# Kernel tuning notes

Hardware: AMD Instinct MI355X
Metric: run time of the kernel (lower is better)

Reference implementation:

```python
import jax, jax.numpy as jnp
import numpy as np
from jax import lax

TAU_REF_HOURS = 1.0
INIT_NOISE_SCALE = 0.01
MAX_GROWTH_RATE = 0.3
B, T, N, D = 2, 64, 512, 256


def setup_inputs() -> dict:
    key = jax.random.key(0)
    ks = jax.random.split(key, 8)
    return {
        "x": jax.random.normal(ks[0], (B, T, N, D), dtype=jnp.float32),
        "dt": jax.random.uniform(ks[1], (B, T), dtype=jnp.float32),
        "eps": jax.random.normal(ks[2], (B, T, N, D), dtype=jnp.float32),
        "u_raw_re": jax.random.normal(ks[3], (D, D), dtype=jnp.float32) * 0.02,
        "u_raw_im": jax.random.normal(ks[4], (D, D), dtype=jnp.float32) * 0.02,
        "lam_re": jax.random.normal(ks[5], (D,), dtype=jnp.float32) * 0.01,
        "lam_im": jax.random.normal(ks[6], (D,), dtype=jnp.float32) * 0.1,
        "noise_raw": jax.random.normal(ks[7], (D,), dtype=jnp.float32) * 0.02,
    }


def reference(x, dt, eps, u_raw_re, u_raw_im, lam_re, lam_im, noise_raw):
    # Unitary basis from QR of complex raw matrix (ComplexSVDTransform._unitary_from_raw)
    u, _ = jnp.linalg.qr(lax.complex(u_raw_re, u_raw_im))  # [D, D] complex

    # encode: x @ conj(u)
    x_enc = jnp.einsum("btnd,de->btne", x.astype(jnp.complex64), jnp.conj(u))

    # effective lambda: lam_re -> -softplus(-lam_re), clamped at -max_growth_rate
    lam_r = jnp.maximum(-jax.nn.softplus(-lam_re), -MAX_GROWTH_RATE)
    lam = lax.complex(lam_r, lam_im)  # [D]

    # continuous decay / forcing operators per (b, t, d)
    exp_arg = (dt / TAU_REF_HOURS)[..., None] * lam  # [B, T, D]
    decay = jnp.exp(exp_arg)
    lam_safe = lam + (1e-8 * jnp.sign(lam_r + 1e-12)).astype(lam.dtype)
    forcing = (decay - 1.0) / lam_safe  # expm1(arg)/lam_safe

    # SDE noise: eps * sqrt(dt) * softplus(noise_raw) * init_noise_scale
    dt_scale = jnp.sqrt(jnp.maximum(dt, 0.0))[:, :, None, None]  # [B,T,1,1]
    n_scale = jax.nn.softplus(noise_raw) * INIT_NOISE_SCALE  # [D]
    noise = eps.astype(jnp.complex64) * (dt_scale * n_scale).astype(jnp.complex64)

    # linear recurrence h_t = decay_t * h_{t-1} + forcing_t * x_enc_t + noise_t
    b_term = forcing[:, :, None, :] * x_enc + noise  # [B,T,N,D]
    a_term = jnp.broadcast_to(decay[:, :, None, :], b_term.shape)

    def combine(e1, e2):
        a1, b1 = e1
        a2, b2 = e2
        return (a2 * a1, a2 * b1 + b2)

    _, h = lax.associative_scan(combine, (a_term, b_term), axis=1)  # [B,T,N,D]

    # decode: h @ u
    y = jnp.einsum("btnd,de->btne", h, u)
    return jnp.stack([y.real, y.imag])  # [2,B,T,N,D] float32
```

## Files before the change

kernel.cpp:

```cpp
#include <hip/hip_runtime.h>
#include <math.h>

#define B_ 2
#define T_ 64
#define N_ 512
#define D_ 256
#define M_ (B_*T_*N_)
#define PLANE ((size_t)M_*D_)

typedef unsigned short u16;
typedef __attribute__((ext_vector_type(8))) short bf16x8;
typedef __attribute__((ext_vector_type(4))) float f32x4;

__device__ __forceinline__ u16 f2bf(float f) {
  union { float f; unsigned u; } cv; cv.f = f;
  unsigned u = cv.u;
  return (u16)((u + 0x7FFFu + ((u >> 16) & 1u)) >> 16);
}
__device__ __forceinline__ float bf2f(u16 h) {
  union { unsigned u; float f; } cv; cv.u = ((unsigned)h) << 16;
  return cv.f;
}

__device__ __forceinline__ float wredsum(float x) {
  x += __uint_as_float(__builtin_amdgcn_update_dpp(0u, __float_as_uint(x), 0x111, 0xf, 0xf, true));
  x += __uint_as_float(__builtin_amdgcn_update_dpp(0u, __float_as_uint(x), 0x112, 0xf, 0xf, true));
  x += __uint_as_float(__builtin_amdgcn_update_dpp(0u, __float_as_uint(x), 0x114, 0xf, 0xf, true));
  x += __uint_as_float(__builtin_amdgcn_update_dpp(0u, __float_as_uint(x), 0x118, 0xf, 0xf, true));
  x += __uint_as_float(__builtin_amdgcn_update_dpp(0u, __float_as_uint(x), 0x142, 0xa, 0xf, true));
  x += __uint_as_float(__builtin_amdgcn_update_dpp(0u, __float_as_uint(x), 0x143, 0xc, 0xf, true));
  return __uint_as_float(__builtin_amdgcn_readlane(__float_as_uint(x), 63));
}
__device__ __forceinline__ float lanebcast(float x, int l) {
  return __uint_as_float(__builtin_amdgcn_readlane(__float_as_uint(x), l));
}

template<int P>
__global__ __launch_bounds__(1024, 1) void qr_megastep(
    const float* __restrict__ ure_raw, const float* __restrict__ uim_raw,
    float2* __restrict__ A, float2* __restrict__ tau)
{
  const int tid = threadIdx.x, lane = tid & 63, w = tid >> 6;
  const int role = blockIdx.x;
  __shared__ float2 sv32[32][256];
  __shared__ float2 sfin[32][256];
  __shared__ float2 snext[2][256];
  __shared__ float2 stau2[2];
  __shared__ float2 stau32[32];
  __shared__ float2 stauOut[32];

  constexpr int J0P  = (P > 0) ? 32*(P-1) : 0;
  constexpr int RP   = 256 - J0P;
  constexpr int MCHP = (RP + 63) >> 6;
  constexpr int PIV  = (P == 0) ? 0 : 32;
  constexpr int J0W  = (P == 0) ? 0 : J0P;
  constexpr int RW   = 256 - J0W;
  constexpr int MCHW = (RW + 63) >> 6;

  if constexpr (P == 0) {
    if (role > 0) {
      const int c0 = 32*role;
      const int c = tid & 31, r0 = tid >> 5;
      #pragma unroll
      for (int r8 = 0; r8 < 8; ++r8) {
        int r = r0 + r8*32;
        A[(size_t)(c0+c)*D_ + r] = make_float2(ure_raw[(size_t)r*D_ + c0 + c],
                                               uim_raw[(size_t)r*D_ + c0 + c]);
      }
      return;
    }
  }

  float2 col[2][4];

  if constexpr (P > 0) {
    #pragma unroll
    for (int it = 0; it < 8; ++it) {
      int idx = it*1024 + tid;
      int c = idx >> 8, rr = idx & 255;
      float2 val = make_float2(0.f, 0.f);
      if (rr < RP) val = A[(size_t)(J0P+c)*D_ + J0P + rr];
      sv32[c][rr] = val;
    }
    if (tid < 32) stau32[tid] = tau[J0P + tid];
    const int c0 = (role > 0) ? 32*(P + role) : 32*P;
    #pragma unroll
    for (int lc = 0; lc < 2; ++lc) {
      int cg = c0 + 2*w + lc;
      #pragma unroll
      for (int m = 0; m < 4; ++m) {
        int rr = m*64 + lane;
        col[lc][m] = make_float2(0.f, 0.f);
        if (m < MCHP && rr < RP) col[lc][m] = A[(size_t)cg*D_ + J0P + rr];
      }
    }
    __syncthreads();

    #pragma unroll 4
    for (int jl = 0; jl < 32; ++jl) {
      float2 tt = stau32[jl];
      float2 v[4];
      { float2 rv = sv32[jl][lane];
        v[0] = (lane > jl) ? rv : ((lane == jl) ? make_float2(1.f, 0.f)
                                                : make_float2(0.f, 0.f)); }
      #pragma unroll
      for (int m = 1; m < 4; ++m) v[m] = sv32[jl][m*64 + lane];
      float wr[2], wi[2];
      #pragma unroll
      for (int lc = 0; lc < 2; ++lc) {
        wr[lc] = 0.f; wi[lc] = 0.f;
        #pragma unroll
        for (int m = 0; m < 4; ++m) {
          if (m < MCHP) {
            float2 a = col[lc][m];
            wr[lc] += v[m].x*a.x + v[m].y*a.y;
            wi[lc] += v[m].x*a.y - v[m].y*a.x;
          }
        }
      }
      #pragma unroll
      for (int lc = 0; lc < 2; ++lc) { wr[lc] = wredsum(wr[lc]);
                                       wi[lc] = wredsum(wi[lc]); }
      #pragma unroll
      for (int lc = 0; lc < 2; ++lc) {
        float fr = tt.x*wr[lc] + tt.y*wi[lc];
        float fi = tt.x*wi[lc] - tt.y*wr[lc];
        #pragma unroll
        for (int m = 0; m < 4; ++m) {
          if (m < MCHP) {
            col[lc][m].x -= fr*v[m].x - fi*v[m].y;
            col[lc][m].y -= fr*v[m].y + fi*v[m].x;
          }
        }
      }
    }

    if (role > 0) {
      #pragma unroll
      for (int lc = 0; lc < 2; ++lc) {
        int cg = 32*(P + role) + 2*w + lc;
        #pragma unroll
        for (int m = 0; m < 4; ++m) {
          int rr = m*64 + lane;
          if (m < MCHP && rr < RP) A[(size_t)cg*D_ + J0P + rr] = col[lc][m];
        }
      }
      return;
    }
    __syncthreads();
  } else {
    #pragma unroll
    for (int lc = 0; lc < 2; ++lc) {
      int cg = 2*w + lc;
      #pragma unroll
      for (int m = 0; m < 4; ++m) {
        int rr = m*64 + lane;
        col[lc][m] = make_float2(ure_raw[(size_t)rr*D_ + cg],
                                 uim_raw[(size_t)rr*D_ + cg]);
      }
    }
  }

  if (w == 0) {
    float part = (lane > PIV) ? (col[0][0].x*col[0][0].x + col[0][0].y*col[0][0].y) : 0.f;
    if (1 < MCHW) part += col[0][1].x*col[0][1].x + col[0][1].y*col[0][1].y;
    if (2 < MCHW) part += col[0][2].x*col[0][2].x + col[0][2].y*col[0][2].y;
    if (3 < MCHW) part += col[0][3].x*col[0][3].x + col[0][3].y*col[0][3].y;
    part = wredsum(part);
    float ar = lanebcast(col[0][0].x, PIV), ai = lanebcast(col[0][0].y, PIV);
    float tr, ti, sr, si, bt;
    if (part == 0.f && ai == 0.f) {
      tr = ti = sr = si = 0.f; bt = ar;
    } else {
      float nrm = sqrtf(ar*ar + ai*ai + part);
      bt = (ar >= 0.f) ? -nrm : nrm;
      tr = (bt - ar)/bt; ti = -ai/bt;
      float dr = ar - bt, di = ai, dn = dr*dr + di*di;
      sr = dr/dn; si = -di/dn;
    }
    if (lane == 0) { stau2[0] = make_float2(tr, ti);
                     stauOut[0] = make_float2(tr, ti); }
    float2 nv0 = make_float2(col[0][0].x*sr - col[0][0].y*si,
                             col[0][0].x*si + col[0][0].y*sr);
    nv0 = (lane > PIV) ? nv0 : ((lane == PIV) ? make_float2(1.f, 0.f)
                                              : make_float2(0.f, 0.f));
    float2 nv1 = make_float2(col[0][1].x*sr - col[0][1].y*si,
                             col[0][1].x*si + col[0][1].y*sr);
    float2 nv2 = make_float2(col[0][2].x*sr - col[0][2].y*si,
                             col[0][2].x*si + col[0][2].y*sr);
    float2 nv3 = make_float2(col[0][3].x*sr - col[0][3].y*si,
                             col[0][3].x*si + col[0][3].y*sr);
    snext[0][lane]       = nv0;
    snext[0][64 + lane]  = nv1;
    snext[0][128 + lane] = nv2;
    snext[0][192 + lane] = nv3;
    float2 o0 = (lane < PIV) ? col[0][0]
              : ((lane == PIV) ? make_float2(bt, 0.f) : nv0);
    sfin[0][lane] = o0;
    if (1 < MCHW) sfin[0][64 + lane]  = nv1;
    if (2 < MCHW) sfin[0][128 + lane] = nv2;
    if (3 < MCHW) sfin[0][192 + lane] = nv3;
  }
  __syncthreads();

  #pragma unroll 1
  for (int jl = 0; jl < 31; ++jl) {
    const int cur = jl & 1, nxt = cur ^ 1;
    float2 v0 = snext[cur][lane],      v1 = snext[cur][64 + lane],
           v2 = snext[cur][128 + lane], v3 = snext[cur][192 + lane];
    float2 tt = stau2[cur];
    #pragma unroll
    for (int lc = 0; lc < 2; ++lc) {
      int cl = 2*w + lc;
      if (cl > jl) {
        float wr, wi;
        { float2 a = col[lc][0];
          wr = v0.x*a.x + v0.y*a.y; wi = v0.x*a.y - v0.y*a.x; }
        if (1 < MCHW) { float2 a = col[lc][1];
          wr += v1.x*a.x + v1.y*a.y; wi += v1.x*a.y - v1.y*a.x; }
        if (2 < MCHW) { float2 a = col[lc][2];
          wr += v2.x*a.x + v2.y*a.y; wi += v2.x*a.y - v2.y*a.x; }
        if (3 < MCHW) { float2 a = col[lc][3];
          wr += v3.x*a.x + v3.y*a.y; wi += v3.x*a.y - v3.y*a.x; }
        wr = wredsum(wr); wi = wredsum(wi);
        float fr = tt.x*wr + tt.y*wi;
        float fi = tt.x*wi - tt.y*wr;
        { col[lc][0].x -= fr*v0.x - fi*v0.y;
          col[lc][0].y -= fr*v0.y + fi*v0.x; }
        if (1 < MCHW) { col[lc][1].x -= fr*v1.x - fi*v1.y;
                        col[lc][1].y -= fr*v1.y + fi*v1.x; }
        if (2 < MCHW) { col[lc][2].x -= fr*v2.x - fi*v2.y;
                        col[lc][2].y -= fr*v2.y + fi*v2.x; }
        if (3 < MCHW) { col[lc][3].x -= fr*v3.x - fi*v3.y;
                        col[lc][3].y -= fr*v3.y + fi*v3.x; }
        if (cl == jl + 1) {
          const int pr = PIV + jl + 1;
          float part = (lane > pr) ? (col[lc][0].x*col[lc][0].x +
                                      col[lc][0].y*col[lc][0].y) : 0.f;
          if (1 < MCHW) part += col[lc][1].x*col[lc][1].x + col[lc][1].y*col[lc][1].y;
          if (2 < MCHW) part += col[lc][2].x*col[lc][2].x + col[lc][2].y*col[lc][2].y;
          if (3 < MCHW) part += col[lc][3].x*col[lc][3].x + col[lc][3].y*col[lc][3].y;
          part = wredsum(part);
          float ar = lanebcast(col[lc][0].x, pr), ai = lanebcast(col[lc][0].y, pr);
          float tr, ti, sr, si, bt;
          if (part == 0.f && ai == 0.f) {
            tr = ti = sr = si = 0.f; bt = ar;
          } else {
            float nrm = sqrtf(ar*ar + ai*ai + part);
            bt = (ar >= 0.f) ? -nrm : nrm;
            tr = (bt - ar)/bt; ti = -ai/bt;
            float dr = ar - bt, di = ai, dn = dr*dr + di*di;
            sr = dr/dn; si = -di/dn;
          }
          if (lane == 0) { stau2[nxt] = make_float2(tr, ti);
                           stauOut[jl+1] = make_float2(tr, ti); }
          float2 m0v = make_float2(col[lc][0].x*sr - col[lc][0].y*si,
                                   col[lc][0].x*si + col[lc][0].y*sr);
          m0v = (lane > pr) ? m0v : ((lane == pr) ? make_float2(1.f, 0.f)
                                                  : make_float2(0.f, 0.f));
          float2 m1v = make_float2(col[lc][1].x*sr - col[lc][1].y*si,
                                   col[lc][1].x*si + col[lc][1].y*sr);
          float2 m2v = make_float2(col[lc][2].x*sr - col[lc][2].y*si,
                                   col[lc][2].x*si + col[lc][2].y*sr);
          float2 m3v = make_float2(col[lc][3].x*sr - col[lc][3].y*si,
                                   col[lc][3].x*si + col[lc][3].y*sr);
          snext[nxt][lane]       = m0v;
          snext[nxt][64 + lane]  = m1v;
          snext[nxt][128 + lane] = m2v;
          snext[nxt][192 + lane] = m3v;
          float2 o0 = (lane < pr) ? col[lc][0]
                    : ((lane == pr) ? make_float2(bt, 0.f) : m0v);
          sfin[jl+1][lane] = o0;
          if (1 < MCHW) sfin[jl+1][64 + lane]  = m1v;
          if (2 < MCHW) sfin[jl+1][128 + lane] = m2v;
          if (3 < MCHW) sfin[jl+1][192 + lane] = m3v;
        }
      }
    }
    __syncthreads();
  }

  #pragma unroll
  for (int it = 0; it < 8; ++it) {
    int idx = it*1024 + tid;
    int c = idx >> 8, rr = idx & 255;
    if (rr < RW) A[(size_t)(32*P + c)*D_ + J0W + rr] = sfin[c][rr];
  }
  if (tid < 32) tau[32*P + tid] = stauOut[tid];
}

__global__ __launch_bounds__(256, 1) void qr_bwd_kernel(
    const float2* __restrict__ A, const float2* __restrict__ tau,
    u16* __restrict__ Benc, u16* __restrict__ Bdec)
{
  const int lane = threadIdx.x & 63;
  const int w = threadIdx.x >> 6;
  const int c = blockIdx.x * 4 + w;
  __shared__ float2 stau[256];
  if (threadIdx.x < 256) stau[threadIdx.x] = tau[threadIdx.x];
  __syncthreads();

  float2 q[4];
  #pragma unroll
  for (int m = 0; m < 4; ++m) {
    q[m] = make_float2(0.f, 0.f);
    if (m*64 + lane == c) q[m].x = 1.f;
  }
  float2 a0[4], a1[4];
  #pragma unroll
  for (int m = 0; m < 4; ++m) a0[m] = A[(size_t)c*D_ + m*64 + lane];
  {
    int i1 = (c >= 1) ? c - 1 : 0;
    #pragma unroll
    for (int m = 0; m < 4; ++m) a1[m] = A[(size_t)i1*D_ + m*64 + lane];
  }

  #pragma unroll 1
  for (int i = c; i >= 0; --i) {
    int ip = (i >= 2) ? i - 2 : 0;
    float2 a2[4];
    #pragma unroll
    for (int m = 0; m < 4; ++m) a2[m] = A[(size_t)ip*D_ + m*64 + lane];

    float2 tt = stau[i];
    float2 v[4];
    #pragma unroll
    for (int m = 0; m < 4; ++m) {
      int r = m*64 + lane;
      v[m] = (r > i) ? a0[m] : ((r == i) ? make_float2(1.f, 0.f)
                                         : make_float2(0.f, 0.f));
    }
    float wr = 0.f, wi = 0.f;
    #pragma unroll
    for (int m = 0; m < 4; ++m) {
      wr += v[m].x*q[m].x + v[m].y*q[m].y;
      wi += v[m].x*q[m].y - v[m].y*q[m].x;
    }
    wr = wredsum(wr); wi = wredsum(wi);
    float fr = tt.x*wr - tt.y*wi;
    float fi = tt.x*wi + tt.y*wr;
    #pragma unroll
    for (int m = 0; m < 4; ++m) {
      q[m].x -= fr*v[m].x - fi*v[m].y;
      q[m].y -= fr*v[m].y + fi*v[m].x;
      a0[m] = a1[m]; a1[m] = a2[m];
    }
  }

  #pragma unroll
  for (int m = 0; m < 4; ++m) {
    int r = m*64 + lane;
    u16 qre = f2bf(q[m].x), qim = f2bf(q[m].y), qimn = f2bf(-q[m].y);
    Benc[(size_t)c*D_ + r]              = qre;
    Benc[(size_t)(c+256)*D_ + r]        = qim;
    Bdec[(size_t)c*512 + r]             = qre;
    Bdec[(size_t)c*512 + 256 + r]       = qimn;
    Bdec[(size_t)(c+256)*512 + r]       = qim;
    Bdec[(size_t)(c+256)*512 + 256 + r] = qre;
  }
}

__global__ __launch_bounds__(256) void coef_kernel(
  const float* __restrict__ dt, const float* __restrict__ lam_re, const float* __restrict__ lam_im,
  const float* __restrict__ noise_raw,
  float* __restrict__ c_dre, float* __restrict__ c_dim, float* __restrict__ c_fre,
  float* __restrict__ c_fim, float* __restrict__ c_ns)
{
  int bt = blockIdx.x; int d = threadIdx.x;
  float dtv = dt[bt];
  float lr = lam_re[d], li = lam_im[d];
  float lam_r = fmaxf(-log1pf(expf(-lr)), -0.3f);
  float ar = dtv*lam_r, ai = dtv*li;
  float er = expf(ar);
  float dre = er*cosf(ai), dim_ = er*sinf(ai);
  float t = lam_r + 1e-12f;
  float sgn = (t > 0.f) ? 1.f : ((t < 0.f) ? -1.f : 0.f);
  float den_re = lam_r + 1e-8f*sgn, den_im = li;
  float nr = dre - 1.f, ni = dim_;
  float d2 = den_re*den_re + den_im*den_im;
  float fre = (nr*den_re + ni*den_im)/d2;
  float fim = (ni*den_re - nr*den_im)/d2;
  float ns = sqrtf(fmaxf(dtv,0.f)) * log1pf(expf(noise_raw[d])) * 0.01f;
  int idx = bt*D_+d;
  c_dre[idx]=dre; c_dim[idx]=dim_; c_fre[idx]=fre; c_fim[idx]=fim; c_ns[idx]=ns;
}

#define LDT 72

__global__ __launch_bounds__(256) void encode_gemm(
    const float* __restrict__ x, const u16* __restrict__ Bt,
    u16* __restrict__ xer16, u16* __restrict__ xei16)
{
  __shared__ u16 sA[128*LDT];
  __shared__ u16 sB[128*LDT];
  const int tid = threadIdx.x;
  const int lane = tid & 63, w = tid >> 6;
  const int wr = w >> 1, wc = w & 1;
  const int l15 = lane & 15, l4 = lane >> 4;
  const int m0 = blockIdx.x * 128;
  const int n0 = blockIdx.y * 128;
  f32x4 acc[4][4] = {};
  for (int kb = 0; kb < 4; ++kb) {
    #pragma unroll
    for (int i = 0; i < 4; ++i) {
      int chunk = i*256 + tid;
      int row = chunk >> 3, k0 = (chunk & 7) * 8;
      const float* xs = x + (size_t)(m0+row)*D_ + kb*64 + k0;
      float4 f0 = *(const float4*)xs;
      float4 f1 = *(const float4*)(xs + 4);
      int4 va;
      va.x = (int)((unsigned)f2bf(f0.x) | ((unsigned)f2bf(f0.y) << 16));
      va.y = (int)((unsigned)f2bf(f0.z) | ((unsigned)f2bf(f0.w) << 16));
      va.z = (int)((unsigned)f2bf(f1.x) | ((unsigned)f2bf(f1.y) << 16));
      va.w = (int)((unsigned)f2bf(f1.z) | ((unsigned)f2bf(f1.w) << 16));
      int4 vb = *(const int4*)(Bt + (size_t)(n0+row)*D_ + kb*64 + k0);
      *(int4*)&sA[row*LDT + k0] = va;
      *(int4*)&sB[row*LDT + k0] = vb;
    }
    __syncthreads();
    #pragma unroll
    for (int ks = 0; ks < 2; ++ks) {
      bf16x8 af[4], bb[4];
      #pragma unroll
      for (int mf = 0; mf < 4; ++mf)
        af[mf] = *(const bf16x8*)&sA[(wr*64 + mf*16 + l15)*LDT + ks*32 + l4*8];
      #pragma unroll
      for (int nf = 0; nf < 4; ++nf)
        bb[nf] = *(const bf16x8*)&sB[(wc*64 + nf*16 + l15)*LDT + ks*32 + l4*8];
      #pragma unroll
      for (int mf = 0; mf < 4; ++mf)
        #pragma unroll
        for (int nf = 0; nf < 4; ++nf)
          acc[mf][nf] = __builtin_amdgcn_mfma_f32_16x16x32_bf16(
              af[mf], bb[nf], acc[mf][nf], 0, 0, 0);
    }
    __syncthreads();
  }
  #pragma unroll
  for (int mf = 0; mf < 4; ++mf)
    #pragma unroll
    for (int nf = 0; nf < 4; ++nf)
      #pragma unroll
      for (int r = 0; r < 4; ++r) {
        int row = m0 + wr*64 + mf*16 + l4*4 + r;
        int col = n0 + wc*64 + nf*16 + l15;
        float v = acc[mf][nf][r];
        if (col < 256) xer16[(size_t)row*D_ + col] = f2bf(v);
        else           xei16[(size_t)row*D_ + col - 256] = f2bf(-v);
      }
}

__global__ __launch_bounds__(256) void decode_gemm(
    const u16* __restrict__ hre16, const u16* __restrict__ him16,
    const u16* __restrict__ Bt, float* __restrict__ out)
{
  __shared__ u16 sA[128*LDT];
  __shared__ u16 sB[128*LDT];
  const int tid = threadIdx.x;
  const int lane = tid & 63, w = tid >> 6;
  const int wr = w >> 1, wc = w & 1;
  const int l15 = lane & 15, l4 = lane >> 4;
  const int m0 = blockIdx.x * 128;
  const int n0 = blockIdx.y * 128;
  f32x4 acc[4][4] = {};
  for (int kb = 0; kb < 8; ++kb) {
    const u16* aplane = (kb < 4) ? hre16 : him16;
    const int kk = (kb & 3) * 64;
    #pragma unroll
    for (int i = 0; i < 4; ++i) {
      int chunk = i*256 + tid;
      int row = chunk >> 3, k0 = (chunk & 7) * 8;
      int4 va = *(const int4*)(aplane + (size_t)(m0+row)*D_ + kk + k0);
      int4 vb = *(const int4*)(Bt + (size_t)(n0+row)*512 + kb*64 + k0);
      *(int4*)&sA[row*LDT + k0] = va;
      *(int4*)&sB[row*LDT + k0] = vb;
    }
    __syncthreads();
    #pragma unroll
    for (int ks = 0; ks < 2; ++ks) {
      bf16x8 af[4], bb[4];
      #pragma unroll
      for (int mf = 0; mf < 4; ++mf)
        af[mf] = *(const bf16x8*)&sA[(wr*64 + mf*16 + l15)*LDT + ks*32 + l4*8];
      #pragma unroll
      for (int nf = 0; nf < 4; ++nf)
        bb[nf] = *(const bf16x8*)&sB[(wc*64 + nf*16 + l15)*LDT + ks*32 + l4*8];
      #pragma unroll
      for (int mf = 0; mf < 4; ++mf)
        #pragma unroll
        for (int nf = 0; nf < 4; ++nf)
          acc[mf][nf] = __builtin_amdgcn_mfma_f32_16x16x32_bf16(
              af[mf], bb[nf], acc[mf][nf], 0, 0, 0);
    }
    __syncthreads();
  }
  #pragma unroll
  for (int mf = 0; mf < 4; ++mf)
    #pragma unroll
    for (int nf = 0; nf < 4; ++nf)
      #pragma unroll
      for (int r = 0; r < 4; ++r) {
        int row = m0 + wr*64 + mf*16 + l4*4 + r;
        int col = n0 + wc*64 + nf*16 + l15;
        float v = acc[mf][nf][r];
        if (col < 256) out[(size_t)row*D_ + col] = v;
        else           out[PLANE + (size_t)row*D_ + col - 256] = v;
      }
}

__global__ __launch_bounds__(256) void scan_kernel(
  const float* __restrict__ eps,
  const float* __restrict__ c_dre, const float* __restrict__ c_dim,
  const float* __restrict__ c_fre, const float* __restrict__ c_fim, const float* __restrict__ c_ns,
  const u16* __restrict__ xer16, const u16* __restrict__ xei16,
  u16* __restrict__ hre16, u16* __restrict__ him16)
{
  int bx = blockIdx.x;
  int b = bx >> 9, n = bx & 511;
  int d = threadIdx.x;
  float hr = 0.f, hi = 0.f;
  for (int t = 0; t < T_; ++t) {
    int bt = b*T_ + t;
    int cidx = bt*D_ + d;
    float dre = c_dre[cidx], dim_ = c_dim[cidx];
    float fre = c_fre[cidx], fim = c_fim[cidx];
    float ns  = c_ns[cidx];
    size_t idx = ((size_t)bt*N_ + n)*D_ + d;
    float xr = bf2f(xer16[idx]), xi = bf2f(xei16[idx]), ep = eps[idx];
    float br = fre*xr - fim*xi + ep*ns;
    float bi = fre*xi + fim*xr;
    float nr2 = dre*hr - dim_*hi + br;
    float ni2 = dre*hi + dim_*hr + bi;
    hr = nr2; hi = ni2;
    hre16[idx] = f2bf(hr); him16[idx] = f2bf(hi);
  }
}

extern "C" void kernel_launch(void* const* d_in, const int* in_sizes, int n_in,
                              void* d_out, int out_size, void* d_ws, size_t ws_size,
                              hipStream_t stream)
{
  const float* x         = (const float*)d_in[0];
  const float* dt        = (const float*)d_in[1];
  const float* eps       = (const float*)d_in[2];
  const float* ure_raw   = (const float*)d_in[3];
  const float* uim_raw   = (const float*)d_in[4];
  const float* lam_re    = (const float*)d_in[5];
  const float* lam_im    = (const float*)d_in[6];
  const float* noise_raw = (const float*)d_in[7];
  float* out = (float*)d_out;

  char* ws = (char*)d_ws;
  float2* A    = (float2*)(ws);
  float2* tau  = (float2*)(ws + 524288);
  u16* Benc    = (u16*)(ws + (1<<20));
  u16* Bdec    = (u16*)(ws + 1572864);
  float* c_dre = (float*)(ws + (2<<20));
  float* c_dim = c_dre + B_*T_*D_;
  float* c_fre = c_dim + B_*T_*D_;
  float* c_fim = c_fre + B_*T_*D_;
  float* c_ns  = c_fim + B_*T_*D_;
  u16* hre16   = (u16*)(ws + ((size_t)4<<20));
  u16* xer16   = (u16*)(ws + ((size_t)36<<20));
  u16* xei16   = (u16*)(ws + ((size_t)68<<20));
  u16* him16   = (u16*)(ws + ((size_t)100<<20));

  qr_megastep<0><<<8, 1024, 0, stream>>>(ure_raw, uim_raw, A, tau);
  qr_megastep<1><<<7, 1024, 0, stream>>>(ure_raw, uim_raw, A, tau);
  qr_megastep<2><<<6, 1024, 0, stream>>>(ure_raw, uim_raw, A, tau);
  qr_megastep<3><<<5, 1024, 0, stream>>>(ure_raw, uim_raw, A, tau);
  qr_megastep<4><<<4, 1024, 0, stream>>>(ure_raw, uim_raw, A, tau);
  qr_megastep<5><<<3, 1024, 0, stream>>>(ure_raw, uim_raw, A, tau);
  qr_megastep<6><<<2, 1024, 0, stream>>>(ure_raw, uim_raw, A, tau);
  qr_megastep<7><<<1, 1024, 0, stream>>>(ure_raw, uim_raw, A, tau);
  qr_bwd_kernel<<<64, 256, 0, stream>>>(A, tau, Benc, Bdec);
  coef_kernel<<<B_*T_, 256, 0, stream>>>(dt, lam_re, lam_im, noise_raw,
                                         c_dre, c_dim, c_fre, c_fim, c_ns);
  encode_gemm<<<dim3(M_/128, 4), 256, 0, stream>>>(x, Benc, xer16, xei16);
  scan_kernel<<<B_*N_, 256, 0, stream>>>(eps, c_dre, c_dim, c_fre, c_fim, c_ns,
                                         xer16, xei16, hre16, him16);
  decode_gemm<<<dim3(M_/128, 4), 256, 0, stream>>>(hre16, him16, Bdec, out);
}
```

Baseline: 737.2 us.

## Apply Householder reflectors two at a time in QR factor and back-accumulation

The panel QR loop now derives two Householder reflectors per step and applies both to the trailing columns with one combined update. The cross term between the two vectors is precomputed, which halves the number of block barriers in the panel factorization. The Q back-accumulation kernel likewise applies two reflectors per iteration, with a prefetch two steps deep. This cuts serial wave reductions and syncs in the QR stages, which are latency-bound. In exchange it adds more registers, more shared memory and a slightly different floating-point rounding order. The QR is a small part of a kernel dominated by the large encode/scan/decode work.

```diff
diff --git a/kernel.cpp b/kernel.cpp
--- a/kernel.cpp
+++ b/kernel.cpp
@@ -44,8 +44,10 @@
   const int role = blockIdx.x;
   __shared__ float2 sv32[32][256];
   __shared__ float2 sfin[32][256];
-  __shared__ float2 snext[2][256];
-  __shared__ float2 stau2[2];
+  __shared__ float2 snA[2][256];
+  __shared__ float2 snB[2][256];
+  __shared__ float4 sscalAB[2];
+  __shared__ float2 sg[2];
   __shared__ float2 stau32[32];
   __shared__ float2 stauOut[32];
 
@@ -161,122 +163,166 @@
     }
   }
 
-  if (w == 0) {
-    float part = (lane > PIV) ? (col[0][0].x*col[0][0].x + col[0][0].y*col[0][0].y) : 0.f;
-    if (1 < MCHW) part += col[0][1].x*col[0][1].x + col[0][1].y*col[0][1].y;
-    if (2 < MCHW) part += col[0][2].x*col[0][2].x + col[0][2].y*col[0][2].y;
-    if (3 < MCHW) part += col[0][3].x*col[0][3].x + col[0][3].y*col[0][3].y;
+  auto derive_pair = [&](float2 (&ca)[4], float2 (&cb)[4], int jlA, int buf) {
+    const int prA = PIV + jlA, prB = prA + 1;
+    float part = (lane > prA) ? (ca[0].x*ca[0].x + ca[0].y*ca[0].y) : 0.f;
+    if (1 < MCHW) part += ca[1].x*ca[1].x + ca[1].y*ca[1].y;
+    if (2 < MCHW) part += ca[2].x*ca[2].x + ca[2].y*ca[2].y;
+    if (3 < MCHW) part += ca[3].x*ca[3].x + ca[3].y*ca[3].y;
     part = wredsum(part);
-    float ar = lanebcast(col[0][0].x, PIV), ai = lanebcast(col[0][0].y, PIV);
-    float tr, ti, sr, si, bt;
+    float ar = lanebcast(ca[0].x, prA), ai = lanebcast(ca[0].y, prA);
+    float trA, tiA, sr, si, btA;
     if (part == 0.f && ai == 0.f) {
-      tr = ti = sr = si = 0.f; bt = ar;
+      trA = tiA = sr = si = 0.f; btA = ar;
     } else {
       float nrm = sqrtf(ar*ar + ai*ai + part);
-      bt = (ar >= 0.f) ? -nrm : nrm;
-      tr = (bt - ar)/bt; ti = -ai/bt;
-      float dr = ar - bt, di = ai, dn = dr*dr + di*di;
+      btA = (ar >= 0.f) ? -nrm : nrm;
+      trA = (btA - ar)/btA; tiA = -ai/btA;
+      float dr = ar - btA, di = ai, dn = dr*dr + di*di;
       sr = dr/dn; si = -di/dn;
     }
-    if (lane == 0) { stau2[0] = make_float2(tr, ti);
-                     stauOut[0] = make_float2(tr, ti); }
-    float2 nv0 = make_float2(col[0][0].x*sr - col[0][0].y*si,
-                             col[0][0].x*si + col[0][0].y*sr);
-    nv0 = (lane > PIV) ? nv0 : ((lane == PIV) ? make_float2(1.f, 0.f)
-                                              : make_float2(0.f, 0.f));
-    float2 nv1 = make_float2(col[0][1].x*sr - col[0][1].y*si,
-                             col[0][1].x*si + col[0][1].y*sr);
-    float2 nv2 = make_float2(col[0][2].x*sr - col[0][2].y*si,
-                             col[0][2].x*si + col[0][2].y*sr);
-    float2 nv3 = make_float2(col[0][3].x*sr - col[0][3].y*si,
-                             col[0][3].x*si + col[0][3].y*sr);
-    snext[0][lane]       = nv0;
-    snext[0][64 + lane]  = nv1;
-    snext[0][128 + lane] = nv2;
-    snext[0][192 + lane] = nv3;
-    float2 o0 = (lane < PIV) ? col[0][0]
-              : ((lane == PIV) ? make_float2(bt, 0.f) : nv0);
-    sfin[0][lane] = o0;
-    if (1 < MCHW) sfin[0][64 + lane]  = nv1;
-    if (2 < MCHW) sfin[0][128 + lane] = nv2;
-    if (3 < MCHW) sfin[0][192 + lane] = nv3;
-  }
+    float2 vA[4];
+    {
+      float2 t0 = make_float2(ca[0].x*sr - ca[0].y*si, ca[0].x*si + ca[0].y*sr);
+      vA[0] = (lane > prA) ? t0 : ((lane == prA) ? make_float2(1.f, 0.f)
+                                                 : make_float2(0.f, 0.f));
+    }
+    vA[1] = make_float2(ca[1].x*sr - ca[1].y*si, ca[1].x*si + ca[1].y*sr);
+    vA[2] = make_float2(ca[2].x*sr - ca[2].y*si, ca[2].x*si + ca[2].y*sr);
+    vA[3] = make_float2(ca[3].x*sr - ca[3].y*si, ca[3].x*si + ca[3].y*sr);
+    {
+      float2 o0 = (lane < prA) ? ca[0]
+                : ((lane == prA) ? make_float2(btA, 0.f) : vA[0]);
+      sfin[jlA][lane] = o0;
+      if (1 < MCHW) sfin[jlA][64 + lane]  = vA[1];
+      if (2 < MCHW) sfin[jlA][128 + lane] = vA[2];
+      if (3 < MCHW) sfin[jlA][192 + lane] = vA[3];
+    }
+    {
+      float wr_ = vA[0].x*cb[0].x + vA[0].y*cb[0].y;
+      float wi_ = vA[0].x*cb[0].y - vA[0].y*cb[0].x;
+      if (1 < MCHW) { wr_ += vA[1].x*cb[1].x + vA[1].y*cb[1].y;
+                      wi_ += vA[1].x*cb[1].y - vA[1].y*cb[1].x; }
+      if (2 < MCHW) { wr_ += vA[2].x*cb[2].x + vA[2].y*cb[2].y;
+                      wi_ += vA[2].x*cb[2].y - vA[2].y*cb[2].x; }
+      if (3 < MCHW) { wr_ += vA[3].x*cb[3].x + vA[3].y*cb[3].y;
+                      wi_ += vA[3].x*cb[3].y - vA[3].y*cb[3].x; }
+      wr_ = wredsum(wr_); wi_ = wredsum(wi_);
+      float fr = trA*wr_ + tiA*wi_;
+      float fi = trA*wi_ - tiA*wr_;
+      cb[0].x -= fr*vA[0].x - fi*vA[0].y; cb[0].y -= fr*vA[0].y + fi*vA[0].x;
+      if (1 < MCHW) { cb[1].x -= fr*vA[1].x - fi*vA[1].y;
+                      cb[1].y -= fr*vA[1].y + fi*vA[1].x; }
+      if (2 < MCHW) { cb[2].x -= fr*vA[2].x - fi*vA[2].y;
+                      cb[2].y -= fr*vA[2].y + fi*vA[2].x; }
+      if (3 < MCHW) { cb[3].x -= fr*vA[3].x - fi*vA[3].y;
+                      cb[3].y -= fr*vA[3].y + fi*vA[3].x; }
+    }
+    float partB = (lane > prB) ? (cb[0].x*cb[0].x + cb[0].y*cb[0].y) : 0.f;
+    if (1 < MCHW) partB += cb[1].x*cb[1].x + cb[1].y*cb[1].y;
+    if (2 < MCHW) partB += cb[2].x*cb[2].x + cb[2].y*cb[2].y;
+    if (3 < MCHW) partB += cb[3].x*cb[3].x + cb[3].y*cb[3].y;
+    partB = wredsum(partB);
+    float br_ = lanebcast(cb[0].x, prB), bi_ = lanebcast(cb[0].y, prB);
+    float trB, tiB, srB, siB, btB;
+    if (partB == 0.f && bi_ == 0.f) {
+      trB = tiB = srB = siB = 0.f; btB = br_;
+    } else {
+      float nrm = sqrtf(br_*br_ + bi_*bi_ + partB);
+      btB = (br_ >= 0.f) ? -nrm : nrm;
+      trB = (btB - br_)/btB; tiB = -bi_/btB;
+      float dr = br_ - btB, di = bi_, dn = dr*dr + di*di;
+      srB = dr/dn; siB = -di/dn;
+    }
+    float2 vB[4];
+    {
+      float2 t0 = make_float2(cb[0].x*srB - cb[0].y*siB, cb[0].x*siB + cb[0].y*srB);
+      vB[0] = (lane > prB) ? t0 : ((lane == prB) ? make_float2(1.f, 0.f)
+                                                 : make_float2(0.f, 0.f));
+    }
+    vB[1] = make_float2(cb[1].x*srB - cb[1].y*siB, cb[1].x*siB + cb[1].y*srB);
+    vB[2] = make_float2(cb[2].x*srB - cb[2].y*siB, cb[2].x*siB + cb[2].y*srB);
+    vB[3] = make_float2(cb[3].x*srB - cb[3].y*siB, cb[3].x*siB + cb[3].y*srB);
+    {
+      float2 o0 = (lane < prB) ? cb[0]
+                : ((lane == prB) ? make_float2(btB, 0.f) : vB[0]);
+      sfin[jlA+1][lane] = o0;
+      if (1 < MCHW) sfin[jlA+1][64 + lane]  = vB[1];
+      if (2 < MCHW) sfin[jlA+1][128 + lane] = vB[2];
+      if (3 < MCHW) sfin[jlA+1][192 + lane] = vB[3];
+    }
+    float gr = vB[0].x*vA[0].x + vB[0].y*vA[0].y;
+    float gi = vB[0].x*vA[0].y - vB[0].y*vA[0].x;
+    if (1 < MCHW) { gr += vB[1].x*vA[1].x + vB[1].y*vA[1].y;
+                    gi += vB[1].x*vA[1].y - vB[1].y*vA[1].x; }
+    if (2 < MCHW) { gr += vB[2].x*vA[2].x + vB[2].y*vA[2].y;
+                    gi += vB[2].x*vA[2].y - vB[2].y*vA[2].x; }
+    if (3 < MCHW) { gr += vB[3].x*vA[3].x + vB[3].y*vA[3].y;
+                    gi += vB[3].x*vA[3].y - vB[3].y*vA[3].x; }
+    gr = wredsum(gr); gi = wredsum(gi);
+    snA[buf][lane] = vA[0]; snA[buf][64+lane] = vA[1];
+    snA[buf][128+lane] = vA[2]; snA[buf][192+lane] = vA[3];
+    snB[buf][lane] = vB[0]; snB[buf][64+lane] = vB[1];
+    snB[buf][128+lane] = vB[2]; snB[buf][192+lane] = vB[3];
+    if (lane == 0) {
+      sscalAB[buf] = make_float4(trA, tiA, trB, tiB);
+      sg[buf] = make_float2(gr, gi);
+      stauOut[jlA]   = make_float2(trA, tiA);
+      stauOut[jlA+1] = make_float2(trB, tiB);
+    }
+  };
+
+  if (w == 0) derive_pair(col[0], col[1], 0, 0);
   __syncthreads();
 
   #pragma unroll 1
-  for (int jl = 0; jl < 31; ++jl) {
-    const int cur = jl & 1, nxt = cur ^ 1;
-    float2 v0 = snext[cur][lane],      v1 = snext[cur][64 + lane],
-           v2 = snext[cur][128 + lane], v3 = snext[cur][192 + lane];
-    float2 tt = stau2[cur];
+  for (int m = 0; m < 15; ++m) {
+    const int cur = m & 1, nxt = cur ^ 1;
+    float2 vA0 = snA[cur][lane],       vA1 = snA[cur][64 + lane],
+           vA2 = snA[cur][128 + lane], vA3 = snA[cur][192 + lane];
+    float2 vB0 = snB[cur][lane],       vB1 = snB[cur][64 + lane],
+           vB2 = snB[cur][128 + lane], vB3 = snB[cur][192 + lane];
+    float4 sc = sscalAB[cur];
+    float2 g  = sg[cur];
     #pragma unroll
     for (int lc = 0; lc < 2; ++lc) {
       int cl = 2*w + lc;
-      if (cl > jl) {
-        float wr, wi;
+      if (cl > 2*m + 1) {
+        float d1r, d1i, d2r, d2i;
         { float2 a = col[lc][0];
-          wr = v0.x*a.x + v0.y*a.y; wi = v0.x*a.y - v0.y*a.x; }
+          d1r = vA0.x*a.x + vA0.y*a.y; d1i = vA0.x*a.y - vA0.y*a.x;
+          d2r = vB0.x*a.x + vB0.y*a.y; d2i = vB0.x*a.y - vB0.y*a.x; }
         if (1 < MCHW) { float2 a = col[lc][1];
-          wr += v1.x*a.x + v1.y*a.y; wi += v1.x*a.y - v1.y*a.x; }
+          d1r += vA1.x*a.x + vA1.y*a.y; d1i += vA1.x*a.y - vA1.y*a.x;
+          d2r += vB1.x*a.x + vB1.y*a.y; d2i += vB1.x*a.y - vB1.y*a.x; }
         if (2 < MCHW) { float2 a = col[lc][2];
-          wr += v2.x*a.x + v2.y*a.y; wi += v2.x*a.y - v2.y*a.x; }
+          d1r += vA2.x*a.x + vA2.y*a.y; d1i += vA2.x*a.y - vA2.y*a.x;
+          d2r += vB2.x*a.x + vB2.y*a.y; d2i += vB2.x*a.y - vB2.y*a.x; }
         if (3 < MCHW) { float2 a = col[lc][3];
-          wr += v3.x*a.x + v3.y*a.y; wi += v3.x*a.y - v3.y*a.x; }
-        wr = wredsum(wr); wi = wredsum(wi);
-        float fr = tt.x*wr + tt.y*wi;
-        float fi = tt.x*wi - tt.y*wr;
-        { col[lc][0].x -= fr*v0.x - fi*v0.y;
-          col[lc][0].y -= fr*v0.y + fi*v0.x; }
-        if (1 < MCHW) { col[lc][1].x -= fr*v1.x - fi*v1.y;
-                        col[lc][1].y -= fr*v1.y + fi*v1.x; }
-        if (2 < MCHW) { col[lc][2].x -= fr*v2.x - fi*v2.y;
-                        col[lc][2].y -= fr*v2.y + fi*v2.x; }
-        if (3 < MCHW) { col[lc][3].x -= fr*v3.x - fi*v3.y;
-                        col[lc][3].y -= fr*v3.y + fi*v3.x; }
-        if (cl == jl + 1) {
-          const int pr = PIV + jl + 1;
-          float part = (lane > pr) ? (col[lc][0].x*col[lc][0].x +
-                                      col[lc][0].y*col[lc][0].y) : 0.f;
-          if (1 < MCHW) part += col[lc][1].x*col[lc][1].x + col[lc][1].y*col[lc][1].y;
-          if (2 < MCHW) part += col[lc][2].x*col[lc][2].x + col[lc][2].y*col[lc][2].y;
-          if (3 < MCHW) part += col[lc][3].x*col[lc][3].x + col[lc][3].y*col[lc][3].y;
-          part = wredsum(part);
-          float ar = lanebcast(col[lc][0].x, pr), ai = lanebcast(col[lc][0].y, pr);
-          float tr, ti, sr, si, bt;
-          if (part == 0.f && ai == 0.f) {
-            tr = ti = sr = si = 0.f; bt = ar;
-          } else {
-            float nrm = sqrtf(ar*ar + ai*ai + part);
-            bt = (ar >= 0.f) ? -nrm : nrm;
-            tr = (bt - ar)/bt; ti = -ai/bt;
-            float dr = ar - bt, di = ai, dn = dr*dr + di*di;
-            sr = dr/dn; si = -di/dn;
-          }
-          if (lane == 0) { stau2[nxt] = make_float2(tr, ti);
-                           stauOut[jl+1] = make_float2(tr, ti); }
-          float2 m0v = make_float2(col[lc][0].x*sr - col[lc][0].y*si,
-                                   col[lc][0].x*si + col[lc][0].y*sr);
-          m0v = (lane > pr) ? m0v : ((lane == pr) ? make_float2(1.f, 0.f)
-                                                  : make_float2(0.f, 0.f));
-          float2 m1v = make_float2(col[lc][1].x*sr - col[lc][1].y*si,
-                                   col[lc][1].x*si + col[lc][1].y*sr);
-          float2 m2v = make_float2(col[lc][2].x*sr - col[lc][2].y*si,
-                                   col[lc][2].x*si + col[lc][2].y*sr);
-          float2 m3v = make_float2(col[lc][3].x*sr - col[lc][3].y*si,
-                                   col[lc][3].x*si + col[lc][3].y*sr);
-          snext[nxt][lane]       = m0v;
-          snext[nxt][64 + lane]  = m1v;
-          snext[nxt][128 + lane] = m2v;
-          snext[nxt][192 + lane] = m3v;
-          float2 o0 = (lane < pr) ? col[lc][0]
-                    : ((lane == pr) ? make_float2(bt, 0.f) : m0v);
-          sfin[jl+1][lane] = o0;
-          if (1 < MCHW) sfin[jl+1][64 + lane]  = m1v;
-          if (2 < MCHW) sfin[jl+1][128 + lane] = m2v;
-          if (3 < MCHW) sfin[jl+1][192 + lane] = m3v;
-        }
-      }
-    }
+          d1r += vA3.x*a.x + vA3.y*a.y; d1i += vA3.x*a.y - vA3.y*a.x;
+          d2r += vB3.x*a.x + vB3.y*a.y; d2i += vB3.x*a.y - vB3.y*a.x; }
+        d1r = wredsum(d1r); d1i = wredsum(d1i);
+        d2r = wredsum(d2r); d2i = wredsum(d2i);
+        float f1r = sc.x*d1r + sc.y*d1i;
+        float f1i = sc.x*d1i - sc.y*d1r;
+        float d2cr = d2r - (f1r*g.x - f1i*g.y);
+        float d2ci = d2i - (f1r*g.y + f1i*g.x);
+        float f2r = sc.z*d2cr + sc.w*d2ci;
+        float f2i = sc.z*d2ci - sc.w*d2cr;
+        { col[lc][0].x -= f1r*vA0.x - f1i*vA0.y + f2r*vB0.x - f2i*vB0.y;
+          col[lc][0].y -= f1r*vA0.y + f1i*vA0.x + f2r*vB0.y + f2i*vB0.x; }
+        if (1 < MCHW) {
+          col[lc][1].x -= f1r*vA1.x - f1i*vA1.y + f2r*vB1.x - f2i*vB1.y;
+          col[lc][1].y -= f1r*vA1.y + f1i*vA1.x + f2r*vB1.y + f2i*vB1.x; }
+        if (2 < MCHW) {
+          col[lc][2].x -= f1r*vA2.x - f1i*vA2.y + f2r*vB2.x - f2i*vB2.y;
+          col[lc][2].y -= f1r*vA2.y + f1i*vA2.x + f2r*vB2.y + f2i*vB2.x; }
+        if (3 < MCHW) {
+          col[lc][3].x -= f1r*vA3.x - f1i*vA3.y + f2r*vB3.x - f2i*vB3.y;
+          col[lc][3].y -= f1r*vA3.y + f1i*vA3.x + f2r*vB3.y + f2i*vB3.x; }
+      }
+    }
+    if (w == m + 1) derive_pair(col[0], col[1], 2*m + 2, nxt);
     __syncthreads();
   }
 
@@ -306,44 +352,89 @@
     q[m] = make_float2(0.f, 0.f);
     if (m*64 + lane == c) q[m].x = 1.f;
   }
-  float2 a0[4], a1[4];
-  #pragma unroll
-  for (int m = 0; m < 4; ++m) a0[m] = A[(size_t)c*D_ + m*64 + lane];
+  float2 A0[4], A1[4], A2[4], A3[4];
   {
-    int i1 = (c >= 1) ? c - 1 : 0;
-    #pragma unroll
-    for (int m = 0; m < 4; ++m) a1[m] = A[(size_t)i1*D_ + m*64 + lane];
-  }
-
+    int i0 = c, i1 = (c >= 1) ? c-1 : 0, i2 = (c >= 2) ? c-2 : 0,
+        i3 = (c >= 3) ? c-3 : 0;
+    #pragma unroll
+    for (int m = 0; m < 4; ++m) {
+      A0[m] = A[(size_t)i0*D_ + m*64 + lane];
+      A1[m] = A[(size_t)i1*D_ + m*64 + lane];
+      A2[m] = A[(size_t)i2*D_ + m*64 + lane];
+      A3[m] = A[(size_t)i3*D_ + m*64 + lane];
+    }
+  }
+
+  int i = c;
   #pragma unroll 1
-  for (int i = c; i >= 0; --i) {
-    int ip = (i >= 2) ? i - 2 : 0;
-    float2 a2[4];
-    #pragma unroll
-    for (int m = 0; m < 4; ++m) a2[m] = A[(size_t)ip*D_ + m*64 + lane];
-
-    float2 tt = stau[i];
-    float2 v[4];
+  while (i >= 1) {
+    float2 ta = stau[i], tb = stau[i-1];
+    float2 vI[4], vJ[4];
     #pragma unroll
     for (int m = 0; m < 4; ++m) {
       int r = m*64 + lane;
-      v[m] = (r > i) ? a0[m] : ((r == i) ? make_float2(1.f, 0.f)
-                                         : make_float2(0.f, 0.f));
+      vI[m] = (r > i)   ? A0[m] : ((r == i)   ? make_float2(1.f, 0.f)
+                                              : make_float2(0.f, 0.f));
+      vJ[m] = (r > i-1) ? A1[m] : ((r == i-1) ? make_float2(1.f, 0.f)
+                                              : make_float2(0.f, 0.f));
+    }
+    float2 P0[4], P1[4];
+    {
+      int n0 = (i >= 4) ? i-4 : 0, n1 = (i >= 5) ? i-5 : 0;
+      #pragma unroll
+      for (int m = 0; m < 4; ++m) {
+        P0[m] = A[(size_t)n0*D_ + m*64 + lane];
+        P1[m] = A[(size_t)n1*D_ + m*64 + lane];
+      }
+    }
+    float d1r = 0.f, d1i = 0.f, d2r = 0.f, d2i = 0.f, gr = 0.f, gi = 0.f;
+    #pragma unroll
+    for (int m = 0; m < 4; ++m) {
+      d1r += vI[m].x*q[m].x + vI[m].y*q[m].y;
+      d1i += vI[m].x*q[m].y - vI[m].y*q[m].x;
+      d2r += vJ[m].x*q[m].x + vJ[m].y*q[m].y;
+      d2i += vJ[m].x*q[m].y - vJ[m].y*q[m].x;
+      gr  += vJ[m].x*vI[m].x + vJ[m].y*vI[m].y;
+      gi  += vJ[m].x*vI[m].y - vJ[m].y*vI[m].x;
+    }
+    d1r = wredsum(d1r); d1i = wredsum(d1i);
+    d2r = wredsum(d2r); d2i = wredsum(d2i);
+    gr  = wredsum(gr);  gi  = wredsum(gi);
+    float f1r = ta.x*d1r - ta.y*d1i;
+    float f1i = ta.x*d1i + ta.y*d1r;
+    float d2cr = d2r - (f1r*gr - f1i*gi);
+    float d2ci = d2i - (f1r*gi + f1i*gr);
+    float f2r = tb.x*d2cr - tb.y*d2ci;
+    float f2i = tb.x*d2ci + tb.y*d2cr;
+    #pragma unroll
+    for (int m = 0; m < 4; ++m) {
+      q[m].x -= f1r*vI[m].x - f1i*vI[m].y + f2r*vJ[m].x - f2i*vJ[m].y;
+      q[m].y -= f1r*vI[m].y + f1i*vI[m].x + f2r*vJ[m].y + f2i*vJ[m].x;
+      A0[m] = A2[m]; A1[m] = A3[m]; A2[m] = P0[m]; A3[m] = P1[m];
+    }
+    i -= 2;
+  }
+  if (i == 0) {
+    float2 tt = stau[0];
+    float2 v0[4];
+    #pragma unroll
+    for (int m = 0; m < 4; ++m) {
+      int r = m*64 + lane;
+      v0[m] = (r > 0) ? A0[m] : make_float2(1.f, 0.f);
     }
     float wr = 0.f, wi = 0.f;
     #pragma unroll
     for (int m = 0; m < 4; ++m) {
-      wr += v[m].x*q[m].x + v[m].y*q[m].y;
-      wi += v[m].x*q[m].y - v[m].y*q[m].x;
+      wr += v0[m].x*q[m].x + v0[m].y*q[m].y;
+      wi += v0[m].x*q[m].y - v0[m].y*q[m].x;
     }
     wr = wredsum(wr); wi = wredsum(wi);
     float fr = tt.x*wr - tt.y*wi;
     float fi = tt.x*wi + tt.y*wr;
     #pragma unroll
     for (int m = 0; m < 4; ++m) {
-      q[m].x -= fr*v[m].x - fi*v[m].y;
-      q[m].y -= fr*v[m].y + fi*v[m].x;
-      a0[m] = a1[m]; a1[m] = a2[m];
+      q[m].x -= fr*v0[m].x - fi*v0[m].y;
+      q[m].y -= fr*v0[m].y + fi*v0[m].x;
     }
   }
 
```

Result: no change. 730.9 us (-0.9%).
